# Optimization experiments

Measured on AMD Instinct MI355X. Metric: run time of the kernel, lower is better.

## Reference

```python
import jax, jax.numpy as jnp
import numpy as np
from jax import lax

IN_CHANNELS = 256
START_SIZE, STOP_SIZE, NUM_WINDOWS = 3, 65, 3
WINDOW_SIZES = np.linspace(START_SIZE, STOP_SIZE, NUM_WINDOWS).round().astype(int).tolist()  # [3, 34, 65]
EPS = 1e-12
NEG_SLOPE = 0.2


def setup_inputs() -> dict:
    key = jax.random.key(0)
    ks = jax.random.split(key, 9)
    N, C, H, W = 2, IN_CHANNELS, 128, 128
    feature = jax.random.normal(ks[0], (N, C, H, W), dtype=jnp.float32)
    c2 = 2 * C  # mean||std concat -> 512
    dims = [(c2, c2 // 2), (c2 // 2, 256), (256, 128), (128, 1)]
    Ws, bs = [], []
    for i, (din, dout) in enumerate(dims):
        Ws.append(jax.random.normal(ks[1 + i], (NUM_WINDOWS, dout, din), dtype=jnp.float32) / np.sqrt(din).astype(np.float32))
        bs.append(jnp.zeros((NUM_WINDOWS, dout), dtype=jnp.float32))
    return {"feature": feature,
            "W1": Ws[0], "b1": bs[0],
            "W2": Ws[1], "b2": bs[1],
            "W3": Ws[2], "b3": bs[2],
            "W4": Ws[3], "b4": bs[3],
            "label": 1}


def _window_stats(feature, K):
    # mean/std over K x K sliding windows, stride (K-1)//2, VALID padding.
    # Equivalent to F.unfold + var_mean(unbiased=False), but via windowed
    # sum / sum-of-squares accumulation (no O(K^2) blow-up).
    s = max(1, (K - 1) // 2)
    wd, ws = (1, 1, K, K), (1, 1, s, s)
    ssum = lax.reduce_window(feature, 0.0, lax.add, wd, ws, 'VALID')
    ssq = lax.reduce_window(feature * feature, 0.0, lax.add, wd, ws, 'VALID')
    n = jnp.float32(K * K)
    mean = ssum / n
    var = jnp.maximum(ssq / n - mean * mean, 0.0)
    std = jnp.sqrt(var + EPS)
    return jnp.concatenate([mean, std], axis=1)  # [N, 2C, NEW_H, NEW_W]


def _mlp(x, W1, b1, W2, b2, W3, b3, W4, b4):
    # x: [N, 2C]; 1x1 convs on a 1x1 spatial map == dense layers
    h = jax.nn.leaky_relu(x @ W1.T + b1, NEG_SLOPE)
    h = jax.nn.leaky_relu(h @ W2.T + b2, NEG_SLOPE)
    h = jax.nn.leaky_relu(h @ W3.T + b3, NEG_SLOPE)
    return h @ W4.T + b4  # [N, 1]


def reference(feature, W1, b1, W2, b2, W3, b3, W4, b4, label):
    y = jnp.float32(label)
    losses = jnp.float32(0.0)
    for i, K in enumerate(WINDOW_SIZES):
        stats = _window_stats(feature, K)          # [N, 2C, h, w]
        pooled = jnp.mean(stats, axis=(2, 3))      # [N, 2C]
        logits = _mlp(pooled, W1[i], b1[i], W2[i], b2[i], W3[i], b3[i], W4[i], b4[i])
        # BCE-with-logits vs constant target y: softplus(l) - l*y, averaged
        losses = losses + jnp.mean(jax.nn.softplus(logits) - logits * y)
    return losses
```

## Files before the change

### kernel.cpp

```cpp
#include <hip/hip_runtime.h>
#include <hip/hip_bf16.h>
#include <math.h>

#define CCH   256
#define HH    128
#define WW    128
#define EPSF  1e-12f
#define EPS81 8.1e-11f
#define SLOPE 0.2f


__device__ __forceinline__ void k3_loadrow(const float* __restrict__ plane, int r, int jb,
                                           float4& rs, float4& rq) {
    const float* rp = &plane[r * WW + jb];
    float4 v = *reinterpret_cast<const float4*>(rp);
    float2 w = *reinterpret_cast<const float2*>(rp + 4);
    float t12 = v.y + v.z, t34 = v.w + w.x;
    rs.x = v.x + t12; rs.y = t12 + v.w; rs.z = v.z + t34; rs.w = t34 + w.y;
    float y0 = v.x * v.x, y1 = v.y * v.y, y2 = v.z * v.z;
    float y3 = v.w * v.w, y4 = w.x * w.x, y5 = w.y * w.y;
    float u12 = y1 + y2, u34 = y3 + y4;
    rq.x = y0 + u12; rq.y = u12 + y3; rq.z = y2 + u34; rq.w = u34 + y5;
}

__device__ __forceinline__ void win_acc(float S, float Q, float wm, float& aS, float& aD) {
    float d = fmaxf(fmaf(S, -S, 9.f * Q), 0.f);
    aS = fmaf(wm, S, aS);
    aD = fmaf(wm, sqrtf(d + EPS81), aD);
}

__global__ __launch_bounds__(512, 4) void stats_kernel(const float* __restrict__ feat,
                                                       float* __restrict__ pooled,
                                                       int N) {
    __shared__ float plane[HH * WW + 8];
    __shared__ float wp[8][6];

    const int p    = blockIdx.x;
    const int n    = p >> 8;
    const int c    = p & 255;
    const int tid  = threadIdx.x;
    const int wave = tid >> 6, lane = tid & 63;

    {
        const float* gbase = feat + (size_t)p * (HH * WW) + (tid << 2);
        #pragma unroll
        for (int i = 0; i < 8; ++i) {
            __builtin_amdgcn_global_load_lds(
                (const __attribute__((address_space(1))) void*)(gbase + i * 2048),
                (__attribute__((address_space(3))) void*)&plane[i * 2048 + (wave << 8)],
                16, 0, 0);
        }
        if (tid < 8) plane[HH * WW + tid] = 0.f;
    }
    __syncthreads();

    float a3S = 0.f, a3D = 0.f;
    {
        const int s  = tid & 31;
        const int g  = tid >> 5;
        const int jb = s << 2;
        const float wm2 = (s < 31) ? 1.f : 0.f;
        const int i0 = g << 3;
        float4 r0s, r0q, r1s, r1q;
        k3_loadrow(plane, i0,     jb, r0s, r0q);
        k3_loadrow(plane, i0 + 1, jb, r1s, r1q);
        #pragma unroll
        for (int t = 0; t < 8; ++t) {
            const int i  = i0 + t;
            const int r2 = (i + 2 < 128) ? (i + 2) : 127;
            float4 r2s, r2q;
            k3_loadrow(plane, r2, jb, r2s, r2q);
            const float wr  = (i < 126) ? 1.f : 0.f;
            const float wrm = wr * wm2;
            float Sx = r0s.x + r1s.x + r2s.x, Qx = r0q.x + r1q.x + r2q.x;
            float Sy = r0s.y + r1s.y + r2s.y, Qy = r0q.y + r1q.y + r2q.y;
            float Sz = r0s.z + r1s.z + r2s.z, Qz = r0q.z + r1q.z + r2q.z;
            float Sw = r0s.w + r1s.w + r2s.w, Qw = r0q.w + r1q.w + r2q.w;
            win_acc(Sx, Qx, wr,  a3S, a3D);
            win_acc(Sy, Qy, wr,  a3S, a3D);
            win_acc(Sz, Qz, wrm, a3S, a3D);
            win_acc(Sw, Qw, wrm, a3S, a3D);
            r0s = r1s; r0q = r1q; r1s = r2s; r1q = r2q;
        }
    }

    float am34 = 0.f, as34 = 0.f;
    for (int w = wave; w < 36; w += 8) {
        int wi = w / 6, wj = w - 6 * wi;
        int r0 = wi << 4, c0 = wj << 4;
        float S = 0.f, Q = 0.f;
        #pragma unroll
        for (int it = 0; it < 5; ++it) {
            int t = lane + (it << 6);
            if (t < 306) {
                int r = t / 9, c4 = t - 9 * r;
                const float* rp = &plane[(r0 + r) * WW + c0 + (c4 << 2)];
                float4 v = *reinterpret_cast<const float4*>(rp);
                if (c4 == 8) { v.z = 0.f; v.w = 0.f; }
                S += (v.x + v.y) + (v.z + v.w);
                Q = fmaf(v.x, v.x, Q); Q = fmaf(v.y, v.y, Q);
                Q = fmaf(v.z, v.z, Q); Q = fmaf(v.w, v.w, Q);
            }
        }
        #pragma unroll
        for (int off = 32; off > 0; off >>= 1) {
            S += __shfl_down(S, off);
            Q += __shfl_down(Q, off);
        }
        if (lane == 0) {
            const float inv = 1.f / 1156.f;
            float mean = S * inv;
            float var  = fmaxf(fmaf(-mean, mean, Q * inv), 0.f);
            am34 += mean;
            as34 += sqrtf(var + EPSF);
        }
    }

    float m65 = 0.f, s65 = 0.f;
    if (wave >= 4) {
        int w  = wave - 4;
        int wi = w >> 1, wj = w & 1;
        int r0 = wi << 5, c0 = wj << 5;
        float S = 0.f, Q = 0.f;
        #pragma unroll
        for (int it = 0; it < 18; ++it) {
            int t = lane + (it << 6);
            if (t < 1105) {
                int r = t / 17, c4 = t - 17 * r;
                const float* rp = &plane[(r0 + r) * WW + c0 + (c4 << 2)];
                float4 v = *reinterpret_cast<const float4*>(rp);
                if (c4 == 16) { v.y = 0.f; v.z = 0.f; v.w = 0.f; }
                S += (v.x + v.y) + (v.z + v.w);
                Q = fmaf(v.x, v.x, Q); Q = fmaf(v.y, v.y, Q);
                Q = fmaf(v.z, v.z, Q); Q = fmaf(v.w, v.w, Q);
            }
        }
        #pragma unroll
        for (int off = 32; off > 0; off >>= 1) {
            S += __shfl_down(S, off);
            Q += __shfl_down(Q, off);
        }
        if (lane == 0) {
            const float inv = 1.f / 4225.f;
            float mean = S * inv;
            float var  = fmaxf(fmaf(-mean, mean, Q * inv), 0.f);
            m65 = mean;
            s65 = sqrtf(var + EPSF);
        }
    }

    #pragma unroll
    for (int off = 32; off > 0; off >>= 1) {
        a3S += __shfl_down(a3S, off);
        a3D += __shfl_down(a3D, off);
    }
    if (lane == 0) {
        wp[wave][0] = a3S; wp[wave][1] = a3D;
        wp[wave][2] = am34; wp[wave][3] = as34;
        wp[wave][4] = m65;  wp[wave][5] = s65;
    }
    __syncthreads();
    if (tid == 0) {
        float A3 = 0.f, D3 = 0.f, M34 = 0.f, S34 = 0.f, M65 = 0.f, S65 = 0.f;
        #pragma unroll
        for (int w = 0; w < 8; ++w) {
            A3 += wp[w][0]; D3 += wp[w][1];
            M34 += wp[w][2]; S34 += wp[w][3];
            M65 += wp[w][4]; S65 += wp[w][5];
        }
        const float inv3 = 1.f / (9.f * 126.f * 126.f);
        pooled[(0 * N + n) * 512 + c]       = A3 * inv3;
        pooled[(0 * N + n) * 512 + 256 + c] = D3 * inv3;
        pooled[(1 * N + n) * 512 + c]       = M34 * (1.f / 36.f);
        pooled[(1 * N + n) * 512 + 256 + c] = S34 * (1.f / 36.f);
        pooled[(2 * N + n) * 512 + c]       = M65 * 0.25f;
        pooled[(2 * N + n) * 512 + 256 + c] = S65 * 0.25f;
    }
}

__device__ __forceinline__ float leaky(float v) { return v > 0.f ? v : SLOPE * v; }

__global__ __launch_bounds__(256) void layer_kernel(const float* __restrict__ W,
                                                    const float* __restrict__ b,
                                                    const float* __restrict__ xin,
                                                    float* __restrict__ xout,
                                                    int DIN, int DOUT, int act) {
    const int wave = threadIdx.x >> 6, lane = threadIdx.x & 63;
    const int r = blockIdx.x * 4 + wave;
    if (r >= 3 * DOUT) return;
    const int k = r / DOUT, o = r - k * DOUT;
    const int DIN4 = DIN >> 2;

    const float4* w4  = reinterpret_cast<const float4*>(W + ((size_t)k * DOUT + o) * DIN);
    const float4* x04 = reinterpret_cast<const float4*>(xin + (size_t)(k * 2 + 0) * DIN);
    const float4* x14 = reinterpret_cast<const float4*>(xin + (size_t)(k * 2 + 1) * DIN);

    float s0 = 0.f, s1 = 0.f;
    for (int j = lane; j < DIN4; j += 64) {
        float4 wv = w4[j], a = x04[j], d = x14[j];
        s0 = fmaf(wv.x, a.x, s0); s0 = fmaf(wv.y, a.y, s0);
        s0 = fmaf(wv.z, a.z, s0); s0 = fmaf(wv.w, a.w, s0);
        s1 = fmaf(wv.x, d.x, s1); s1 = fmaf(wv.y, d.y, s1);
        s1 = fmaf(wv.z, d.z, s1); s1 = fmaf(wv.w, d.w, s1);
    }
    #pragma unroll
    for (int off = 32; off > 0; off >>= 1) {
        s0 += __shfl_down(s0, off);
        s1 += __shfl_down(s1, off);
    }
    if (lane == 0) {
        float bb = b[k * DOUT + o];
        float v0 = s0 + bb, v1 = s1 + bb;
        if (act) { v0 = leaky(v0); v1 = leaky(v1); }
        xout[(size_t)(k * 2 + 0) * DOUT + o] = v0;
        xout[(size_t)(k * 2 + 1) * DOUT + o] = v1;
    }
}

__global__ __launch_bounds__(384) void final_kernel(const float* __restrict__ W4,
                                                    const float* __restrict__ b4,
                                                    const float* __restrict__ h3,
                                                    const int* __restrict__ label,
                                                    float* __restrict__ out) {
    __shared__ float lossArr[6];
    const int wave = threadIdx.x >> 6, lane = threadIdx.x & 63;
    {
        const int k = wave >> 1, n = wave & 1;
        const float* w = &W4[(size_t)k * 128];
        const float* x = &h3[(size_t)(k * 2 + n) * 128];
        float s = w[lane] * x[lane] + w[lane + 64] * x[lane + 64];
        #pragma unroll
        for (int off = 32; off > 0; off >>= 1) s += __shfl_down(s, off);
        if (lane == 0) {
            float logit = s + b4[k];
            float y = (float)(*label);
            float sp = fmaxf(logit, 0.f) + log1pf(expf(-fabsf(logit)));
            lossArr[wave] = sp - logit * y;
        }
    }
    __syncthreads();
    if (threadIdx.x == 0) {
        float tot = 0.f;
        #pragma unroll
        for (int k = 0; k < 3; ++k)
            tot += (lossArr[k * 2 + 0] + lossArr[k * 2 + 1]) * 0.5f;
        out[0] = tot;
    }
}

extern "C" void kernel_launch(void* const* d_in, const int* in_sizes, int n_in,
                              void* d_out, int out_size, void* d_ws, size_t ws_size,
                              hipStream_t stream) {
    const float* feat = (const float*)d_in[0];
    const float* W1   = (const float*)d_in[1];
    const float* b1   = (const float*)d_in[2];
    const float* W2   = (const float*)d_in[3];
    const float* b2   = (const float*)d_in[4];
    const float* W3   = (const float*)d_in[5];
    const float* b3   = (const float*)d_in[6];
    const float* W4   = (const float*)d_in[7];
    const float* b4   = (const float*)d_in[8];
    const int* label  = (const int*)d_in[9];

    const int N = in_sizes[0] / (CCH * HH * WW);

    float* pooled = (float*)d_ws;
    float* h1     = pooled + (size_t)3 * N * 512;
    float* h2     = h1     + (size_t)3 * N * 256;
    float* h3     = h2     + (size_t)3 * N * 256;

    stats_kernel<<<N * CCH, 512, 0, stream>>>(feat, pooled, N);

    layer_kernel<<<192, 256, 0, stream>>>(W1, b1, pooled, h1, 512, 256, 1);
    layer_kernel<<<192, 256, 0, stream>>>(W2, b2, h1, h2, 256, 256, 1);
    layer_kernel<<<96, 256, 0, stream>>>(W3, b3, h2, h3, 256, 128, 1);
    final_kernel<<<1, 384, 0, stream>>>(W4, b4, h3, label, (float*)d_out);
}
```

Before: 33.75 us.

## Fuse MLP layers into one cooperative kernel with grid-wide syncs

Replaces the four separate MLP launches (three dense layers plus the final loss kernel) with a single cooperative kernel that uses grid.sync between layers. The aim is to remove per-launch overhead and the gaps between small dependent kernels. The cost is grid-wide barrier latency, and the code hardcodes N=2 indexing. The old launches remain as a fallback if the cooperative launch fails.

```diff
diff --git a/kernel.cpp b/kernel.cpp
--- a/kernel.cpp
+++ b/kernel.cpp
@@ -1,6 +1,9 @@
 #include <hip/hip_runtime.h>
 #include <hip/hip_bf16.h>
+#include <hip/hip_cooperative_groups.h>
 #include <math.h>
+
+namespace cg = cooperative_groups;
 
 #define CCH   256
 #define HH    128
@@ -180,6 +183,146 @@
 
 __device__ __forceinline__ float leaky(float v) { return v > 0.f ? v : SLOPE * v; }
 
+__global__ __launch_bounds__(256) void mlp_all(const float* __restrict__ pooled,
+                                               const float* __restrict__ W1, const float* __restrict__ b1,
+                                               const float* __restrict__ W2, const float* __restrict__ b2,
+                                               const float* __restrict__ W3, const float* __restrict__ b3,
+                                               const float* __restrict__ W4, const float* __restrict__ b4,
+                                               const int* __restrict__ label,
+                                               float* __restrict__ h1,
+                                               float* __restrict__ h2,
+                                               float* __restrict__ h3,
+                                               float* __restrict__ out) {
+    cg::grid_group grid = cg::this_grid();
+    __shared__ float lossArr[6];
+    const int tid  = threadIdx.x;
+    const int wave = tid >> 6, lane = tid & 63;
+    const int gw   = blockIdx.x * 4 + wave;
+
+    #pragma unroll
+    for (int rr = 0; rr < 2; ++rr) {
+        const int r = gw * 2 + rr;
+        const int k = r >> 8, o = r & 255;
+        const float4* w4  = reinterpret_cast<const float4*>(W1 + ((size_t)k * 256 + o) * 512);
+        const float4* x04 = reinterpret_cast<const float4*>(pooled + (size_t)(k * 2 + 0) * 512);
+        const float4* x14 = reinterpret_cast<const float4*>(pooled + (size_t)(k * 2 + 1) * 512);
+        float4 wa = w4[lane], wb = w4[lane + 64];
+        float4 xa = x04[lane], xb = x04[lane + 64];
+        float4 ya = x14[lane], yb = x14[lane + 64];
+        float s0 = 0.f, s1 = 0.f;
+        s0 = fmaf(wa.x, xa.x, s0); s0 = fmaf(wa.y, xa.y, s0);
+        s0 = fmaf(wa.z, xa.z, s0); s0 = fmaf(wa.w, xa.w, s0);
+        s0 = fmaf(wb.x, xb.x, s0); s0 = fmaf(wb.y, xb.y, s0);
+        s0 = fmaf(wb.z, xb.z, s0); s0 = fmaf(wb.w, xb.w, s0);
+        s1 = fmaf(wa.x, ya.x, s1); s1 = fmaf(wa.y, ya.y, s1);
+        s1 = fmaf(wa.z, ya.z, s1); s1 = fmaf(wa.w, ya.w, s1);
+        s1 = fmaf(wb.x, yb.x, s1); s1 = fmaf(wb.y, yb.y, s1);
+        s1 = fmaf(wb.z, yb.z, s1); s1 = fmaf(wb.w, yb.w, s1);
+        #pragma unroll
+        for (int off = 32; off > 0; off >>= 1) {
+            s0 += __shfl_down(s0, off);
+            s1 += __shfl_down(s1, off);
+        }
+        if (lane == 0) {
+            float bb = b1[k * 256 + o];
+            h1[(size_t)(k * 2 + 0) * 256 + o] = leaky(s0 + bb);
+            h1[(size_t)(k * 2 + 1) * 256 + o] = leaky(s1 + bb);
+        }
+    }
+    __threadfence();
+    grid.sync();
+
+    #pragma unroll
+    for (int rr = 0; rr < 2; ++rr) {
+        const int r = gw * 2 + rr;
+        const int k = r >> 8, o = r & 255;
+        const float4* w4  = reinterpret_cast<const float4*>(W2 + ((size_t)k * 256 + o) * 256);
+        const float4* x04 = reinterpret_cast<const float4*>(h1 + (size_t)(k * 2 + 0) * 256);
+        const float4* x14 = reinterpret_cast<const float4*>(h1 + (size_t)(k * 2 + 1) * 256);
+        float4 wa = w4[lane];
+        float4 xa = x04[lane];
+        float4 ya = x14[lane];
+        float s0 = 0.f, s1 = 0.f;
+        s0 = fmaf(wa.x, xa.x, s0); s0 = fmaf(wa.y, xa.y, s0);
+        s0 = fmaf(wa.z, xa.z, s0); s0 = fmaf(wa.w, xa.w, s0);
+        s1 = fmaf(wa.x, ya.x, s1); s1 = fmaf(wa.y, ya.y, s1);
+        s1 = fmaf(wa.z, ya.z, s1); s1 = fmaf(wa.w, ya.w, s1);
+        #pragma unroll
+        for (int off = 32; off > 0; off >>= 1) {
+            s0 += __shfl_down(s0, off);
+            s1 += __shfl_down(s1, off);
+        }
+        if (lane == 0) {
+            float bb = b2[k * 256 + o];
+            h2[(size_t)(k * 2 + 0) * 256 + o] = leaky(s0 + bb);
+            h2[(size_t)(k * 2 + 1) * 256 + o] = leaky(s1 + bb);
+        }
+    }
+    __threadfence();
+    grid.sync();
+
+    {
+        const int r = gw;
+        const int k = r >> 7, o = r & 127;
+        const float4* w4  = reinterpret_cast<const float4*>(W3 + ((size_t)k * 128 + o) * 256);
+        const float4* x04 = reinterpret_cast<const float4*>(h2 + (size_t)(k * 2 + 0) * 256);
+        const float4* x14 = reinterpret_cast<const float4*>(h2 + (size_t)(k * 2 + 1) * 256);
+        float4 wa = w4[lane];
+        float4 xa = x04[lane];
+        float4 ya = x14[lane];
+        float s0 = 0.f, s1 = 0.f;
+        s0 = fmaf(wa.x, xa.x, s0); s0 = fmaf(wa.y, xa.y, s0);
+        s0 = fmaf(wa.z, xa.z, s0); s0 = fmaf(wa.w, xa.w, s0);
+        s1 = fmaf(wa.x, ya.x, s1); s1 = fmaf(wa.y, ya.y, s1);
+        s1 = fmaf(wa.z, ya.z, s1); s1 = fmaf(wa.w, ya.w, s1);
+        #pragma unroll
+        for (int off = 32; off > 0; off >>= 1) {
+            s0 += __shfl_down(s0, off);
+            s1 += __shfl_down(s1, off);
+        }
+        if (lane == 0) {
+            float bb = b3[k * 128 + o];
+            h3[(size_t)(k * 2 + 0) * 128 + o] = leaky(s0 + bb);
+            h3[(size_t)(k * 2 + 1) * 128 + o] = leaky(s1 + bb);
+        }
+    }
+    __threadfence();
+    grid.sync();
+
+    if (blockIdx.x == 0) {
+        #pragma unroll
+        for (int pr = 0; pr < 2; ++pr) {
+            const int pair = wave + pr * 4;
+            if (pair < 6) {
+                const int k = pair >> 1;
+                float s = 0.f;
+                if (lane < 32) {
+                    float4 wv = reinterpret_cast<const float4*>(W4 + (size_t)k * 128)[lane];
+                    float4 hv = reinterpret_cast<const float4*>(h3 + (size_t)pair * 128)[lane];
+                    s = fmaf(wv.x, hv.x, s); s = fmaf(wv.y, hv.y, s);
+                    s = fmaf(wv.z, hv.z, s); s = fmaf(wv.w, hv.w, s);
+                }
+                #pragma unroll
+                for (int off = 32; off > 0; off >>= 1) s += __shfl_down(s, off);
+                if (lane == 0) {
+                    float logit = s + b4[k];
+                    float y = (float)(*label);
+                    float sp = fmaxf(logit, 0.f) + log1pf(expf(-fabsf(logit)));
+                    lossArr[pair] = sp - logit * y;
+                }
+            }
+        }
+        __syncthreads();
+        if (tid == 0) {
+            float tot = 0.f;
+            #pragma unroll
+            for (int k = 0; k < 3; ++k)
+                tot += (lossArr[k * 2 + 0] + lossArr[k * 2 + 1]) * 0.5f;
+            out[0] = tot;
+        }
+    }
+}
+
 __global__ __launch_bounds__(256) void layer_kernel(const float* __restrict__ W,
                                                     const float* __restrict__ b,
                                                     const float* __restrict__ xin,
@@ -268,11 +411,26 @@
     float* h1     = pooled + (size_t)3 * N * 512;
     float* h2     = h1     + (size_t)3 * N * 256;
     float* h3     = h2     + (size_t)3 * N * 256;
+    float* outp   = (float*)d_out;
 
     stats_kernel<<<N * CCH, 512, 0, stream>>>(feat, pooled, N);
 
-    layer_kernel<<<192, 256, 0, stream>>>(W1, b1, pooled, h1, 512, 256, 1);
-    layer_kernel<<<192, 256, 0, stream>>>(W2, b2, h1, h2, 256, 256, 1);
-    layer_kernel<<<96, 256, 0, stream>>>(W3, b3, h2, h3, 256, 128, 1);
-    final_kernel<<<1, 384, 0, stream>>>(W4, b4, h3, label, (float*)d_out);
-}
+    void* kargs[] = {
+        (void*)&pooled,
+        (void*)&W1, (void*)&b1,
+        (void*)&W2, (void*)&b2,
+        (void*)&W3, (void*)&b3,
+        (void*)&W4, (void*)&b4,
+        (void*)&label,
+        (void*)&h1, (void*)&h2, (void*)&h3,
+        (void*)&outp,
+    };
+    hipError_t err = hipLaunchCooperativeKernel((const void*)mlp_all, dim3(96), dim3(256),
+                                                kargs, 0, stream);
+    if (err != hipSuccess) {
+        layer_kernel<<<192, 256, 0, stream>>>(W1, b1, pooled, h1, 512, 256, 1);
+        layer_kernel<<<192, 256, 0, stream>>>(W2, b2, h1, h2, 256, 256, 1);
+        layer_kernel<<<96, 256, 0, stream>>>(W3, b3, h2, h3, 256, 128, 1);
+        final_kernel<<<1, 384, 0, stream>>>(W4, b4, h3, label, (float*)d_out);
+    }
+}
```

New measurement: 99.56 us. 2.95x slower.

## Fuse layer3 with final loss via atomic last-block, widen stats blocks to 1024

Applied to the files above, without the earlier changes.

Merges the third MLP layer and the final BCE kernel into one launch. An agent-scope atomic counter lets the last-finishing block compute the logits and loss. The stats kernel now uses 1024 threads per plane, halving per-thread rows and loads, and resets the counter. This removes one kernel launch and adds parallelism per plane, at the cost of atomic/fence overhead and different occupancy.

```diff
diff --git a/kernel.cpp b/kernel.cpp
--- a/kernel.cpp
+++ b/kernel.cpp
@@ -29,11 +29,12 @@
     aD = fmaf(wm, sqrtf(d + EPS81), aD);
 }
 
-__global__ __launch_bounds__(512, 4) void stats_kernel(const float* __restrict__ feat,
-                                                       float* __restrict__ pooled,
-                                                       int N) {
+__global__ __launch_bounds__(1024, 4) void stats_kernel(const float* __restrict__ feat,
+                                                        float* __restrict__ pooled,
+                                                        int* __restrict__ bar,
+                                                        int N) {
     __shared__ float plane[HH * WW + 8];
-    __shared__ float wp[8][6];
+    __shared__ float wp[16][6];
 
     const int p    = blockIdx.x;
     const int n    = p >> 8;
@@ -41,13 +42,15 @@
     const int tid  = threadIdx.x;
     const int wave = tid >> 6, lane = tid & 63;
 
+    if (p == 0 && tid < 8) bar[tid] = 0;
+
     {
         const float* gbase = feat + (size_t)p * (HH * WW) + (tid << 2);
         #pragma unroll
-        for (int i = 0; i < 8; ++i) {
+        for (int i = 0; i < 4; ++i) {
             __builtin_amdgcn_global_load_lds(
-                (const __attribute__((address_space(1))) void*)(gbase + i * 2048),
-                (__attribute__((address_space(3))) void*)&plane[i * 2048 + (wave << 8)],
+                (const __attribute__((address_space(1))) void*)(gbase + i * 4096),
+                (__attribute__((address_space(3))) void*)&plane[i * 4096 + (wave << 8)],
                 16, 0, 0);
         }
         if (tid < 8) plane[HH * WW + tid] = 0.f;
@@ -60,12 +63,12 @@
         const int g  = tid >> 5;
         const int jb = s << 2;
         const float wm2 = (s < 31) ? 1.f : 0.f;
-        const int i0 = g << 3;
+        const int i0 = g << 2;
         float4 r0s, r0q, r1s, r1q;
         k3_loadrow(plane, i0,     jb, r0s, r0q);
-        k3_loadrow(plane, i0 + 1, jb, r1s, r1q);
-        #pragma unroll
-        for (int t = 0; t < 8; ++t) {
+        k3_loadrow(plane, (i0 + 1 < 128) ? i0 + 1 : 127, jb, r1s, r1q);
+        #pragma unroll
+        for (int t = 0; t < 4; ++t) {
             const int i  = i0 + t;
             const int r2 = (i + 2 < 128) ? (i + 2) : 127;
             float4 r2s, r2q;
@@ -85,7 +88,7 @@
     }
 
     float am34 = 0.f, as34 = 0.f;
-    for (int w = wave; w < 36; w += 8) {
+    for (int w = wave; w < 36; w += 16) {
         int wi = w / 6, wj = w - 6 * wi;
         int r0 = wi << 4, c0 = wj << 4;
         float S = 0.f, Q = 0.f;
@@ -117,7 +120,7 @@
     }
 
     float m65 = 0.f, s65 = 0.f;
-    if (wave >= 4) {
+    if (wave >= 4 && wave < 8) {
         int w  = wave - 4;
         int wi = w >> 1, wj = w & 1;
         int r0 = wi << 5, c0 = wj << 5;
@@ -163,7 +166,7 @@
     if (tid == 0) {
         float A3 = 0.f, D3 = 0.f, M34 = 0.f, S34 = 0.f, M65 = 0.f, S65 = 0.f;
         #pragma unroll
-        for (int w = 0; w < 8; ++w) {
+        for (int w = 0; w < 16; ++w) {
             A3 += wp[w][0]; D3 += wp[w][1];
             M34 += wp[w][2]; S34 += wp[w][3];
             M65 += wp[w][4]; S65 += wp[w][5];
@@ -217,34 +220,88 @@
     }
 }
 
-__global__ __launch_bounds__(384) void final_kernel(const float* __restrict__ W4,
+__global__ __launch_bounds__(256) void layer3_final(const float* __restrict__ W3,
+                                                    const float* __restrict__ b3,
+                                                    const float* __restrict__ h2,
+                                                    float* __restrict__ h3,
+                                                    const float* __restrict__ W4,
                                                     const float* __restrict__ b4,
-                                                    const float* __restrict__ h3,
                                                     const int* __restrict__ label,
+                                                    int* __restrict__ bar,
                                                     float* __restrict__ out) {
     __shared__ float lossArr[6];
-    const int wave = threadIdx.x >> 6, lane = threadIdx.x & 63;
+    __shared__ int   winner;
+    const int tid  = threadIdx.x;
+    const int wave = tid >> 6, lane = tid & 63;
+    const int r = blockIdx.x * 4 + wave;
+
     {
-        const int k = wave >> 1, n = wave & 1;
-        const float* w = &W4[(size_t)k * 128];
-        const float* x = &h3[(size_t)(k * 2 + n) * 128];
-        float s = w[lane] * x[lane] + w[lane + 64] * x[lane + 64];
-        #pragma unroll
-        for (int off = 32; off > 0; off >>= 1) s += __shfl_down(s, off);
+        const int k = r >> 7, o = r & 127;
+        const float4* w4  = reinterpret_cast<const float4*>(W3 + ((size_t)k * 128 + o) * 256);
+        const float4* x04 = reinterpret_cast<const float4*>(h2 + (size_t)(k * 2 + 0) * 256);
+        const float4* x14 = reinterpret_cast<const float4*>(h2 + (size_t)(k * 2 + 1) * 256);
+        float4 wa = w4[lane];
+        float4 xa = x04[lane];
+        float4 ya = x14[lane];
+        float s0 = 0.f, s1 = 0.f;
+        s0 = fmaf(wa.x, xa.x, s0); s0 = fmaf(wa.y, xa.y, s0);
+        s0 = fmaf(wa.z, xa.z, s0); s0 = fmaf(wa.w, xa.w, s0);
+        s1 = fmaf(wa.x, ya.x, s1); s1 = fmaf(wa.y, ya.y, s1);
+        s1 = fmaf(wa.z, ya.z, s1); s1 = fmaf(wa.w, ya.w, s1);
+        #pragma unroll
+        for (int off = 32; off > 0; off >>= 1) {
+            s0 += __shfl_down(s0, off);
+            s1 += __shfl_down(s1, off);
+        }
         if (lane == 0) {
-            float logit = s + b4[k];
-            float y = (float)(*label);
-            float sp = fmaxf(logit, 0.f) + log1pf(expf(-fabsf(logit)));
-            lossArr[wave] = sp - logit * y;
-        }
-    }
+            float bb = b3[(size_t)k * 128 + o];
+            h3[(size_t)(k * 2 + 0) * 128 + o] = leaky(s0 + bb);
+            h3[(size_t)(k * 2 + 1) * 128 + o] = leaky(s1 + bb);
+        }
+    }
+
     __syncthreads();
-    if (threadIdx.x == 0) {
-        float tot = 0.f;
-        #pragma unroll
-        for (int k = 0; k < 3; ++k)
-            tot += (lossArr[k * 2 + 0] + lossArr[k * 2 + 1]) * 0.5f;
-        out[0] = tot;
+    if (tid == 0) {
+        __threadfence();
+        int prev = __hip_atomic_fetch_add(&bar[0], 1, __ATOMIC_ACQ_REL,
+                                          __HIP_MEMORY_SCOPE_AGENT);
+        winner = (prev == 95) ? 1 : 0;
+    }
+    __syncthreads();
+    if (winner) {
+        __threadfence();
+        if (wave < 4) {
+            #pragma unroll
+            for (int pr = 0; pr < 2; ++pr) {
+                const int pair = wave + pr * 4;
+                if (pair < 6) {
+                    const int k = pair >> 1;
+                    float s = 0.f;
+                    if (lane < 32) {
+                        float4 wv = reinterpret_cast<const float4*>(W4 + (size_t)k * 128)[lane];
+                        float4 hv = reinterpret_cast<const float4*>(h3 + (size_t)pair * 128)[lane];
+                        s = fmaf(wv.x, hv.x, s); s = fmaf(wv.y, hv.y, s);
+                        s = fmaf(wv.z, hv.z, s); s = fmaf(wv.w, hv.w, s);
+                    }
+                    #pragma unroll
+                    for (int off = 32; off > 0; off >>= 1) s += __shfl_down(s, off);
+                    if (lane == 0) {
+                        float logit = s + b4[k];
+                        float y = (float)(*label);
+                        float sp = fmaxf(logit, 0.f) + log1pf(expf(-fabsf(logit)));
+                        lossArr[pair] = sp - logit * y;
+                    }
+                }
+            }
+        }
+        __syncthreads();
+        if (tid == 0) {
+            float tot = 0.f;
+            #pragma unroll
+            for (int k = 0; k < 3; ++k)
+                tot += (lossArr[k * 2 + 0] + lossArr[k * 2 + 1]) * 0.5f;
+            out[0] = tot;
+        }
     }
 }
 
@@ -268,11 +325,12 @@
     float* h1     = pooled + (size_t)3 * N * 512;
     float* h2     = h1     + (size_t)3 * N * 256;
     float* h3     = h2     + (size_t)3 * N * 256;
-
-    stats_kernel<<<N * CCH, 512, 0, stream>>>(feat, pooled, N);
+    int*   bar    = (int*)(h3 + (size_t)3 * N * 128);
+
+    stats_kernel<<<N * CCH, 1024, 0, stream>>>(feat, pooled, bar, N);
 
     layer_kernel<<<192, 256, 0, stream>>>(W1, b1, pooled, h1, 512, 256, 1);
     layer_kernel<<<192, 256, 0, stream>>>(W2, b2, h1, h2, 256, 256, 1);
-    layer_kernel<<<96, 256, 0, stream>>>(W3, b3, h2, h3, 256, 128, 1);
-    final_kernel<<<1, 384, 0, stream>>>(W4, b4, h3, label, (float*)d_out);
-}
+    layer3_final<<<96, 256, 0, stream>>>(W3, b3, h2, h3, W4, b4, label, bar,
+                                         (float*)d_out);
+}
```

Result: slower. 38.29 us (+13.5%).
